# Kernel optimization log

Measured on AMD Instinct MI355X. Metric: run time of the kernel, lower is better.

## Reference

```python
import jax, jax.numpy as jnp
import numpy as np

H = 64   # hidden_size
N = 128  # input_size (num nodes)
B = 64   # batch
T = 96   # seq_len
LN_EPS = 1e-5


def setup_inputs() -> dict:
    key = jax.random.key(0)
    ks = jax.random.split(key, 4)
    x = jax.random.normal(ks[0], (B, T, N), jnp.float32)
    # xavier_uniform-like scale for per-node gate weights [N, 1+H, 4H]
    lim = float(np.sqrt(6.0 / ((1 + H) + 4 * H)))
    w = jax.random.uniform(ks[1], (N, 1 + H, 4 * H), jnp.float32, -lim, lim)
    b = jnp.zeros((N, 4 * H), jnp.float32)
    ln_g = jnp.ones((H,), jnp.float32)
    ln_b = jnp.zeros((H,), jnp.float32)
    fc_w = jax.random.normal(ks[2], (1, H), jnp.float32) * (1.0 / np.sqrt(H))
    fc_b = jnp.zeros((1,), jnp.float32)
    return {"x": x, "w": w, "b": b, "ln_g": ln_g, "ln_b": ln_b,
            "fc_w": fc_w, "fc_b": fc_b}


def _crelu(z):
    return jnp.maximum(z.real, 0) + 1j * jnp.maximum(z.imag, 0)


def _csigmoid(z):
    # torch.sigmoid on complex: 1/(1+exp(-z))
    return 1.0 / (1.0 + jnp.exp(-z))


def _fc_att(x, pool_axes):
    # adaptive_avg_pool to 1 over pool_axes, (C)ReLU, sigmoid, rescale
    squeeze = jnp.mean(x, axis=pool_axes, keepdims=True)
    if jnp.iscomplexobj(x):
        exc = _crelu(squeeze)
        return x * _csigmoid(exc)
    exc = jnp.maximum(squeeze, 0)
    return x * jax.nn.sigmoid(exc)


def reference(x, w, b, ln_g, ln_b, fc_w, fc_b):
    Bb, Tt, Nn = x.shape
    h0 = jnp.zeros((Bb, Nn, H), x.dtype)
    c0 = jnp.zeros((Bb, Nn, H), x.dtype)

    def step(carry, x_t):  # x_t: [B, N]
        h, c = carry
        comb = jnp.concatenate([x_t[..., None], h], axis=-1)      # [B,N,1+H]
        gates = jnp.einsum('bni,nio->bno', comb, w) + b            # [B,N,4H]
        i_g, f_g, o_g, c_tilda = jnp.split(gates, 4, axis=-1)
        # NOTE: original cell does NOT apply tanh to c_tilda
        c_new = jax.nn.sigmoid(f_g) * c + jax.nn.sigmoid(i_g) * c_tilda
        h_new = jax.nn.sigmoid(o_g) * jnp.tanh(c_new)
        return (h_new, c_new), h_new

    _, hs = jax.lax.scan(step, (h0, c0), jnp.swapaxes(x, 0, 1))    # [T,B,N,H]
    lstm_out = jnp.sum(hs, axis=0)                                  # sum over time -> [B,N,H]

    # inter_op: FFT pairwise interaction over the node axis
    m = jnp.fft.rfft(lstm_out, axis=1, norm='ortho')                # [B,F,H] complex, F=N//2+1
    x_f = m[:, :, None, :] * m[:, None, :, :]                       # [B,F,F,H]
    x_f = _fc_att(x_f, (2, 3))
    x_f = jnp.sum(x_f, axis=1)                                      # [B,F,H]
    n_out = 2 * (x_f.shape[1] - 1)                                  # torch irfft default n
    feats = jnp.fft.irfft(x_f, n=n_out, axis=1, norm='ortho')       # [B,N,H] real
    feats = _fc_att(feats, (2,))
    out = jnp.sum(feats, axis=1)                                    # [B,H]

    # LayerNorm(H) -> Linear(H,1) -> sigmoid
    mu = jnp.mean(out, axis=-1, keepdims=True)
    var = jnp.var(out, axis=-1, keepdims=True)
    out = (out - mu) / jnp.sqrt(var + LN_EPS) * ln_g + ln_b
    out = out @ fc_w.T + fc_b                                       # [B,1]
    return jax.nn.sigmoid(out)
```

## Files before the change

kernel.cpp:

```cpp
#include <hip/hip_runtime.h>
#include <math.h>

#define T_STEPS 96
#define N_NODES 128
#define B_SZ 64
#define H_SZ 64

typedef __attribute__((ext_vector_type(8))) __bf16 bf16x8;
typedef __attribute__((ext_vector_type(4))) float f32x4;

__device__ __forceinline__ float rcp_fast(float x){ return __builtin_amdgcn_rcpf(x); }
__device__ __forceinline__ float exp2_fast(float x){ return __builtin_amdgcn_exp2f(x); }
__device__ __forceinline__ float sigm(float v){ return rcp_fast(1.0f + __expf(-v)); }

__global__ __launch_bounds__(256, 2) void lstm_kernel(
    const float* __restrict__ x, const float* __restrict__ w,
    const float* __restrict__ bias, float* __restrict__ yout)
{
  __shared__ __align__(16) unsigned short hb[2][16*72];
  __shared__ float xsl[T_STEPS*16];

  const int n   = blockIdx.x >> 2;
  const int bq  = blockIdx.x & 3;
  const int tid = threadIdx.x;
  const int wv  = tid >> 6;
  const int ln  = tid & 63;
  const int l15 = ln & 15;
  const int q   = ln >> 4;

  for (int i = tid; i < 2*16*72; i += 256) ((unsigned short*)hb)[i] = 0;
  for (int i = tid; i < T_STEPS*16; i += 256){
    int t2 = i >> 4, bl = i & 15;
    xsl[i] = x[(bq*16 + bl)*(T_STEPS*N_NODES) + t2*N_NODES + n];
  }

  const float LOG2E = 1.4426950408889634f;
  const float* wn = w + n*(65*256);

  bf16x8 aF[4][2];
  f32x4 w04[4], bg4[4];
#pragma unroll
  for (int g = 0; g < 4; ++g){
    const float sc = (g < 3) ? LOG2E : 1.0f;
    const int colA = g*64 + wv*16 + l15;
#pragma unroll
    for (int ks = 0; ks < 2; ++ks)
#pragma unroll
      for (int j = 0; j < 8; ++j)
        aF[g][ks][j] = (__bf16)(wn[(1 + ks*32 + q*8 + j)*256 + colA] * sc);
#pragma unroll
    for (int r = 0; r < 4; ++r){
      const int colD = g*64 + wv*16 + q*4 + r;
      w04[g][r] = wn[colD] * sc;
      bg4[g][r] = bias[n*256 + colD] * sc;
    }
  }

  f32x4 cv  = {0.f,0.f,0.f,0.f};
  f32x4 hsv = {0.f,0.f,0.f,0.f};
  __syncthreads();

#pragma unroll 2
  for (int t = 0; t < T_STEPS; ++t){
    const unsigned short* cur = hb[t & 1];
    unsigned short*       nxt = (unsigned short*)hb[(t & 1) ^ 1];

    bf16x8 b0 = *(const bf16x8*)&cur[l15*72 +  0 + q*8];
    bf16x8 b1 = *(const bf16x8*)&cur[l15*72 + 32 + q*8];
    float xv = xsl[t*16 + l15];

    f32x4 acc[4];
#pragma unroll
    for (int g = 0; g < 4; ++g){
      f32x4 a = w04[g]*xv + bg4[g];
      a = __builtin_amdgcn_mfma_f32_16x16x32_bf16(aF[g][0], b0, a, 0,0,0);
      a = __builtin_amdgcn_mfma_f32_16x16x32_bf16(aF[g][1], b1, a, 0,0,0);
      acc[g] = a;
    }

    f32x4 sI, sF, sO, th;
#pragma unroll
    for (int r = 0; r < 4; ++r){
      sI[r] = rcp_fast(1.0f + exp2_fast(-acc[0][r]));
      sF[r] = rcp_fast(1.0f + exp2_fast(-acc[1][r]));
      sO[r] = rcp_fast(1.0f + exp2_fast(-acc[2][r]));
    }
    cv = sF*cv + sI*acc[3];
#pragma unroll
    for (int r = 0; r < 4; ++r){
      float e = exp2_fast(cv[r]*2.8853900817779268f);
      th[r] = fmaf(-2.0f, rcp_fast(e + 1.0f), 1.0f);
    }
    f32x4 hn = sO*th;
    hsv += hn;

    ushort4 pk;
    pk.x = __builtin_bit_cast(unsigned short, (__bf16)hn[0]);
    pk.y = __builtin_bit_cast(unsigned short, (__bf16)hn[1]);
    pk.z = __builtin_bit_cast(unsigned short, (__bf16)hn[2]);
    pk.w = __builtin_bit_cast(unsigned short, (__bf16)hn[3]);
    *(ushort4*)&nxt[l15*72 + wv*16 + q*4] = pk;
    __syncthreads();
  }

  float4 o4 = {hsv[0], hsv[1], hsv[2], hsv[3]};
  *(float4*)&yout[((bq*16 + l15)*N_NODES + n)*H_SZ + wv*16 + q*4] = o4;
}

__global__ __launch_bounds__(256, 2) void dft_kernel(
    const float* __restrict__ y, float* __restrict__ Mout)
{
  __shared__ __align__(16) float ysl[128*20];
  __shared__ float twc[128], tws[128];
  const int b   = blockIdx.x >> 2;
  const int hg  = blockIdx.x & 3;
  const int tid = threadIdx.x;

  if (tid < 128){
    float ang = (float)((double)tid * 0.04908738521234052);
    twc[tid] = cosf(ang);
    tws[tid] = sinf(ang);
  }
  for (int i = tid; i < 128*16; i += 256){
    int nn = i >> 4, h = i & 15;
    ysl[nn*20 + h] = y[(b*N_NODES + nn)*H_SZ + hg*16 + h];
  }
  __syncthreads();

  for (int o = tid; o < 65*4; o += 256){
    int k  = o >> 2;
    int hq = o & 3;
    float re0=0,re1=0,re2=0,re3=0,im0=0,im1=0,im2=0,im3=0;
    for (int nn = 0; nn < 128; ++nn){
      float4 yv = *(const float4*)&ysl[nn*20 + hq*4];
      int j = (k*nn) & 127;
      float cc = twc[j], ss = tws[j];
      re0 = fmaf(yv.x, cc, re0); im0 = fmaf(yv.x, -ss, im0);
      re1 = fmaf(yv.y, cc, re1); im1 = fmaf(yv.y, -ss, im1);
      re2 = fmaf(yv.z, cc, re2); im2 = fmaf(yv.z, -ss, im2);
      re3 = fmaf(yv.w, cc, re3); im3 = fmaf(yv.w, -ss, im3);
    }
    const float s = 0.08838834764831845f;
    const int hb2 = hg*16 + hq*4;
    float* mre = Mout + ((b*2+0)*65 + k)*H_SZ + hb2;
    float* mim = Mout + ((b*2+1)*65 + k)*H_SZ + hb2;
    mre[0]=re0*s; mre[1]=re1*s; mre[2]=re2*s; mre[3]=re3*s;
    mim[0]=im0*s; mim[1]=im1*s; mim[2]=im2*s; mim[3]=im3*s;
  }
}

__global__ __launch_bounds__(256, 1) void post_kernel(
    const float* __restrict__ y, const float* __restrict__ Mws,
    const float* __restrict__ ln_g, const float* __restrict__ ln_b,
    const float* __restrict__ fc_w, const float* __restrict__ fc_b,
    float* __restrict__ out)
{
  __shared__ float ysh[128*65];
  __shared__ float Mre[65*65];
  __shared__ float Mim[65*65];
  __shared__ float twc[128], tws[128];
  __shared__ float Sre[64], Sim[64];
  __shared__ float gr[65], gi[65];
  __shared__ float Gre[64], Gim[64];
  __shared__ float att[128];
  __shared__ float PQ[65*2], AA[65*2];
  __shared__ float outv[64];

  const int b   = blockIdx.x;
  const int tid = threadIdx.x;

  if (tid < 128){
    float ang = (float)((double)tid * 0.04908738521234052);
    twc[tid] = cosf(ang);
    tws[tid] = sinf(ang);
  }
  for (int i = tid; i < 128*16; i += 256){
    int nn = i >> 4, h4 = (i & 15)*4;
    float4 v = *(const float4*)&y[(b*N_NODES + nn)*H_SZ + h4];
    ysh[nn*65 + h4+0] = v.x; ysh[nn*65 + h4+1] = v.y;
    ysh[nn*65 + h4+2] = v.z; ysh[nn*65 + h4+3] = v.w;
  }
  for (int i = tid; i < 65*16; i += 256){
    int k = i >> 4, h4 = (i & 15)*4;
    float4 vr = *(const float4*)&Mws[((b*2+0)*65 + k)*H_SZ + h4];
    float4 vi = *(const float4*)&Mws[((b*2+1)*65 + k)*H_SZ + h4];
    Mre[k*65 + h4+0] = vr.x; Mre[k*65 + h4+1] = vr.y;
    Mre[k*65 + h4+2] = vr.z; Mre[k*65 + h4+3] = vr.w;
    Mim[k*65 + h4+0] = vi.x; Mim[k*65 + h4+1] = vi.y;
    Mim[k*65 + h4+2] = vi.z; Mim[k*65 + h4+3] = vi.w;
  }
  __syncthreads();

  if (tid < 64){
    float sr=0, si=0;
    for (int k = 0; k < 65; ++k){ sr += Mre[k*65+tid]; si += Mim[k*65+tid]; }
    Sre[tid]=sr; Sim[tid]=si;
  }
  __syncthreads();

  if (tid < 65){
    float a=0, bb=0;
    for (int h = 0; h < 64; ++h){
      float mr = Mre[tid*65+h], mi = Mim[tid*65+h];
      a  += mr*Sre[h] - mi*Sim[h];
      bb += mr*Sim[h] + mi*Sre[h];
    }
    a  *= (1.0f/4160.0f);  bb *= (1.0f/4160.0f);
    a = fmaxf(a, 0.0f);    bb = fmaxf(bb, 0.0f);
    float t  = __expf(-a);
    float cb = cosf(bb), sb = sinf(bb);
    float dre = 1.0f + t*cb;
    float dim = t*sb;
    float nrm = rcp_fast(dre*dre + dim*dim);
    gr[tid] = dre*nrm;
    gi[tid] = dim*nrm;
  }
  __syncthreads();

  if (tid < 64){
    float grh=0, gih=0;
    for (int k = 0; k < 65; ++k){
      float mr = Mre[k*65+tid], mi = Mim[k*65+tid];
      float gk = gr[k], hk = gi[k];
      grh += gk*mr - hk*mi;
      gih += gk*mi + hk*mr;
    }
    Gre[tid]=grh; Gim[tid]=gih;
  }
  __syncthreads();

  if (tid < 65){
    float p=0, qq=0;
    for (int h = 0; h < 64; ++h){
      float gimh = Gim[h];
      p  += gimh * Mim[tid*65+h];
      qq += gimh * Mre[tid*65+h];
    }
    const float s2 = 2.0f*0.08838834764831845f;
    PQ[tid*2]   = p*s2;
    PQ[tid*2+1] = qq*s2;
  }
  __syncthreads();

  if (tid < 128){
    float u=0;
    for (int h = 0; h < 64; ++h) u += Gre[h]*ysh[tid*65+h];
    float v=0;
    for (int k = 1; k < 64; ++k){
      int j = (k*tid) & 127;
      v += PQ[k*2]*twc[j] + PQ[k*2+1]*tws[j];
    }
    float mean = (u - v)*(1.0f/64.0f);
    att[tid] = sigm(fmaxf(mean, 0.0f));
  }
  __syncthreads();

  if (tid < 65){
    float ac=0, as=0;
    for (int nn = 0; nn < 128; ++nn){
      int j = (tid*nn) & 127;
      float a2 = att[nn];
      ac = fmaf(a2, twc[j], ac);
      as = fmaf(a2, tws[j], as);
    }
    const float s2 = 2.0f*0.08838834764831845f;
    AA[tid*2]   = ac*s2;
    AA[tid*2+1] = as*s2;
  }
  __syncthreads();

  if (tid < 64){
    float wyh=0;
    for (int nn = 0; nn < 128; ++nn) wyh += att[nn]*ysh[nn*65+tid];
    float wHh=0;
    for (int k = 1; k < 64; ++k)
      wHh += Mim[k*65+tid]*AA[k*2] + Mre[k*65+tid]*AA[k*2+1];
    outv[tid] = Gre[tid]*wyh - Gim[tid]*wHh;
  }
  __syncthreads();

  if (tid < 64){
    float o = outv[tid];
    float s = o;
    for (int off = 32; off; off >>= 1) s += __shfl_xor(s, off, 64);
    float mu = s*(1.0f/64.0f);
    float d  = o - mu;
    float vv = d*d;
    for (int off = 32; off; off >>= 1) vv += __shfl_xor(vv, off, 64);
    float var = vv*(1.0f/64.0f);
    float zo = (d / sqrtf(var + 1e-5f))*ln_g[tid] + ln_b[tid];
    float z  = zo * fc_w[tid];
    for (int off = 32; off; off >>= 1) z += __shfl_xor(z, off, 64);
    if (tid == 0) out[b] = 1.0f/(1.0f + __expf(-(z + fc_b[0])));
  }
}

extern "C" void kernel_launch(void* const* d_in, const int* in_sizes, int n_in,
                              void* d_out, int out_size, void* d_ws, size_t ws_size,
                              hipStream_t stream) {
  (void)in_sizes; (void)n_in; (void)out_size; (void)ws_size;
  const float* x    = (const float*)d_in[0];
  const float* w    = (const float*)d_in[1];
  const float* bia  = (const float*)d_in[2];
  const float* ln_g = (const float*)d_in[3];
  const float* ln_b = (const float*)d_in[4];
  const float* fc_w = (const float*)d_in[5];
  const float* fc_b = (const float*)d_in[6];
  float* out = (float*)d_out;

  float* y = (float*)d_ws;
  float* M = y + (size_t)B_SZ*N_NODES*H_SZ;

  lstm_kernel<<<dim3(512), dim3(256), 0, stream>>>(x, w, bia, y);
  dft_kernel <<<dim3(256), dim3(256), 0, stream>>>(y, M);
  post_kernel<<<dim3(64),  dim3(256), 0, stream>>>(y, M, ln_g, ln_b, fc_w, fc_b, out);
}
```

Baseline: 165.6 us.

## Run each LSTM recurrence in a single wave, folding input and bias into MFMA

The LSTM kernel now uses one 64-thread wave per (node, batch-quarter) task, and that wave computes all 16 gate tiles. This removes the per-timestep __syncthreads and the double-buffered hidden state, which a single wave can read and write in place. The x·w0 and bias terms move into a third MFMA, using a split-bf16 hi/lo trick to keep precision. The gate math is fused to use fewer reciprocals, and the tanh input is clamped. In exchange each wave does six times more serial MFMA and elementwise work per step, and fewer waves are active across the GPU.

Result: slower. 230.4 us (+39.1%).

```diff
diff --git a/kernel.cpp b/kernel.cpp
--- a/kernel.cpp
+++ b/kernel.cpp
@@ -13,23 +13,22 @@
 __device__ __forceinline__ float exp2_fast(float x){ return __builtin_amdgcn_exp2f(x); }
 __device__ __forceinline__ float sigm(float v){ return rcp_fast(1.0f + __expf(-v)); }
 
-__global__ __launch_bounds__(256, 2) void lstm_kernel(
+__global__ __launch_bounds__(64, 1) void lstm_kernel(
     const float* __restrict__ x, const float* __restrict__ w,
     const float* __restrict__ bias, float* __restrict__ yout)
 {
-  __shared__ __align__(16) unsigned short hb[2][16*72];
+  __shared__ __align__(16) unsigned short hsh[16*72];
   __shared__ float xsl[T_STEPS*16];
 
-  const int n   = blockIdx.x >> 2;
-  const int bq  = blockIdx.x & 3;
-  const int tid = threadIdx.x;
-  const int wv  = tid >> 6;
-  const int ln  = tid & 63;
-  const int l15 = ln & 15;
-  const int q   = ln >> 4;
-
-  for (int i = tid; i < 2*16*72; i += 256) ((unsigned short*)hb)[i] = 0;
-  for (int i = tid; i < T_STEPS*16; i += 256){
+  const int task = blockIdx.x;
+  const int bq   = task >> 7;
+  const int n    = task & 127;
+  const int tid  = threadIdx.x;
+  const int l15  = tid & 15;
+  const int q    = tid >> 4;
+
+  for (int i = tid; i < 16*72; i += 64) hsh[i] = 0;
+  for (int i = tid; i < T_STEPS*16; i += 64){
     int t2 = i >> 4, bl = i & 15;
     xsl[i] = x[(bq*16 + bl)*(T_STEPS*N_NODES) + t2*N_NODES + n];
   }
@@ -37,74 +36,100 @@
   const float LOG2E = 1.4426950408889634f;
   const float* wn = w + n*(65*256);
 
-  bf16x8 aF[4][2];
-  f32x4 w04[4], bg4[4];
+  bf16x8 aF[16][2];
+  bf16x8 a2[16];
 #pragma unroll
   for (int g = 0; g < 4; ++g){
     const float sc = (g < 3) ? LOG2E : 1.0f;
-    const int colA = g*64 + wv*16 + l15;
-#pragma unroll
-    for (int ks = 0; ks < 2; ++ks)
-#pragma unroll
-      for (int j = 0; j < 8; ++j)
-        aF[g][ks][j] = (__bf16)(wn[(1 + ks*32 + q*8 + j)*256 + colA] * sc);
-#pragma unroll
-    for (int r = 0; r < 4; ++r){
-      const int colD = g*64 + wv*16 + q*4 + r;
-      w04[g][r] = wn[colD] * sc;
-      bg4[g][r] = bias[n*256 + colD] * sc;
-    }
-  }
-
-  f32x4 cv  = {0.f,0.f,0.f,0.f};
-  f32x4 hsv = {0.f,0.f,0.f,0.f};
-  __syncthreads();
-
-#pragma unroll 2
+#pragma unroll
+    for (int hg = 0; hg < 4; ++hg){
+      const int tl  = g*4 + hg;
+      const int col = g*64 + hg*16 + l15;
+#pragma unroll
+      for (int ks = 0; ks < 2; ++ks)
+#pragma unroll
+        for (int j = 0; j < 8; ++j)
+          aF[tl][ks][j] = (__bf16)(wn[(1 + ks*32 + q*8 + j)*256 + col] * sc);
+      bf16x8 av;
+#pragma unroll
+      for (int j = 0; j < 8; ++j) av[j] = (__bf16)0.0f;
+      if (q == 0){
+        float w0 = wn[col] * sc;
+        __bf16 w0h = (__bf16)w0;
+        av[0] = w0h;
+        av[1] = (__bf16)(bias[n*256 + col] * sc);
+        av[2] = w0h;
+        av[3] = (__bf16)(w0 - (float)w0h);
+      }
+      a2[tl] = av;
+    }
+  }
+
+  f32x4 c4[4], hs4[4];
+#pragma unroll
+  for (int hg = 0; hg < 4; ++hg){
+    c4[hg]  = (f32x4){0.f,0.f,0.f,0.f};
+    hs4[hg] = (f32x4){0.f,0.f,0.f,0.f};
+  }
+  __syncthreads();
+
+#pragma unroll 1
   for (int t = 0; t < T_STEPS; ++t){
-    const unsigned short* cur = hb[t & 1];
-    unsigned short*       nxt = (unsigned short*)hb[(t & 1) ^ 1];
-
-    bf16x8 b0 = *(const bf16x8*)&cur[l15*72 +  0 + q*8];
-    bf16x8 b1 = *(const bf16x8*)&cur[l15*72 + 32 + q*8];
+    bf16x8 b0 = *(const bf16x8*)&hsh[l15*72 +  0 + q*8];
+    bf16x8 b1 = *(const bf16x8*)&hsh[l15*72 + 32 + q*8];
     float xv = xsl[t*16 + l15];
-
-    f32x4 acc[4];
-#pragma unroll
-    for (int g = 0; g < 4; ++g){
-      f32x4 a = w04[g]*xv + bg4[g];
-      a = __builtin_amdgcn_mfma_f32_16x16x32_bf16(aF[g][0], b0, a, 0,0,0);
-      a = __builtin_amdgcn_mfma_f32_16x16x32_bf16(aF[g][1], b1, a, 0,0,0);
-      acc[g] = a;
-    }
-
-    f32x4 sI, sF, sO, th;
-#pragma unroll
-    for (int r = 0; r < 4; ++r){
-      sI[r] = rcp_fast(1.0f + exp2_fast(-acc[0][r]));
-      sF[r] = rcp_fast(1.0f + exp2_fast(-acc[1][r]));
-      sO[r] = rcp_fast(1.0f + exp2_fast(-acc[2][r]));
-    }
-    cv = sF*cv + sI*acc[3];
-#pragma unroll
-    for (int r = 0; r < 4; ++r){
-      float e = exp2_fast(cv[r]*2.8853900817779268f);
-      th[r] = fmaf(-2.0f, rcp_fast(e + 1.0f), 1.0f);
-    }
-    f32x4 hn = sO*th;
-    hsv += hn;
-
-    ushort4 pk;
-    pk.x = __builtin_bit_cast(unsigned short, (__bf16)hn[0]);
-    pk.y = __builtin_bit_cast(unsigned short, (__bf16)hn[1]);
-    pk.z = __builtin_bit_cast(unsigned short, (__bf16)hn[2]);
-    pk.w = __builtin_bit_cast(unsigned short, (__bf16)hn[3]);
-    *(ushort4*)&nxt[l15*72 + wv*16 + q*4] = pk;
-    __syncthreads();
-  }
-
-  float4 o4 = {hsv[0], hsv[1], hsv[2], hsv[3]};
-  *(float4*)&yout[((bq*16 + l15)*N_NODES + n)*H_SZ + wv*16 + q*4] = o4;
+    __bf16 xh = (__bf16)xv;
+    __bf16 xl = (__bf16)(xv - (float)xh);
+    bf16x8 b2;
+#pragma unroll
+    for (int j = 0; j < 8; ++j) b2[j] = (__bf16)0.0f;
+    if (q == 0){ b2[0] = xh; b2[1] = (__bf16)1.0f; b2[2] = xl; b2[3] = xh; }
+
+    f32x4 acc[16];
+#pragma unroll
+    for (int tl = 0; tl < 16; ++tl){
+      f32x4 a = {0.f,0.f,0.f,0.f};
+      a = __builtin_amdgcn_mfma_f32_16x16x32_bf16(aF[tl][0], b0, a, 0,0,0);
+      a = __builtin_amdgcn_mfma_f32_16x16x32_bf16(aF[tl][1], b1, a, 0,0,0);
+      a = __builtin_amdgcn_mfma_f32_16x16x32_bf16(a2[tl],   b2, a, 0,0,0);
+      acc[tl] = a;
+    }
+
+#pragma unroll
+    for (int hg = 0; hg < 4; ++hg){
+      f32x4 cv = c4[hg];
+      f32x4 hn;
+#pragma unroll
+      for (int r = 0; r < 4; ++r){
+        float gi = acc[0*4+hg][r], gf = acc[1*4+hg][r];
+        float go = acc[2*4+hg][r], ct = acc[3*4+hg][r];
+        float ei = exp2_fast(-gi), ef = exp2_fast(-gf);
+        float pf = 1.0f + ef, pi = 1.0f + ei;
+        float num = fmaf(cv[r], ei, cv[r]);
+        num = fmaf(ct, pf, num);
+        float cn = num * rcp_fast(pf*pi);
+        cv[r] = cn;
+        float eo = exp2_fast(-go);
+        float ea = fminf(cn*2.8853900817779268f, 126.0f);
+        float ec = exp2_fast(ea);
+        hn[r] = (ec - 1.0f) * rcp_fast((1.0f + eo)*(ec + 1.0f));
+      }
+      c4[hg]   = cv;
+      hs4[hg] += hn;
+      ushort4 pk;
+      pk.x = __builtin_bit_cast(unsigned short, (__bf16)hn[0]);
+      pk.y = __builtin_bit_cast(unsigned short, (__bf16)hn[1]);
+      pk.z = __builtin_bit_cast(unsigned short, (__bf16)hn[2]);
+      pk.w = __builtin_bit_cast(unsigned short, (__bf16)hn[3]);
+      *(ushort4*)&hsh[l15*72 + hg*16 + q*4] = pk;
+    }
+  }
+
+#pragma unroll
+  for (int hg = 0; hg < 4; ++hg){
+    float4 o4 = {hs4[hg][0], hs4[hg][1], hs4[hg][2], hs4[hg][3]};
+    *(float4*)&yout[((bq*16 + l15)*N_NODES + n)*H_SZ + hg*16 + q*4] = o4;
+  }
 }
 
 __global__ __launch_bounds__(256, 2) void dft_kernel(
@@ -311,7 +336,7 @@
   float* y = (float*)d_ws;
   float* M = y + (size_t)B_SZ*N_NODES*H_SZ;
 
-  lstm_kernel<<<dim3(512), dim3(256), 0, stream>>>(x, w, bia, y);
+  lstm_kernel<<<dim3(512), dim3(64),  0, stream>>>(x, w, bia, y);
   dft_kernel <<<dim3(256), dim3(256), 0, stream>>>(y, M);
   post_kernel<<<dim3(64),  dim3(256), 0, stream>>>(y, M, ln_g, ln_b, fc_w, fc_b, out);
 }
```

## Split LSTM recurrence across 8 waves with gate-interleaved MFMA rows

Applied to the files above, without the earlier changes.

Doubles the LSTM block to 512 threads so each wave owns 8 hidden units. The weight rows are permuted so that one MFMA output tile holds all four gates (i, f, o, c~) of a hidden unit in a single lane's accumulator. This halves the MFMAs per wave on the serial per-timestep critical path. It also fuses the sigmoid/tanh math so that one reciprocal covers the combined gate denominators, cutting transcendental ops. In exchange, barrier synchronisation now spans 8 waves, occupancy pressure rises, and the final output stores become scalar.

New measurement: 172.1 us. +3.9%, slower.

```diff
diff --git a/kernel.cpp b/kernel.cpp
--- a/kernel.cpp
+++ b/kernel.cpp
@@ -13,7 +13,7 @@
 __device__ __forceinline__ float exp2_fast(float x){ return __builtin_amdgcn_exp2f(x); }
 __device__ __forceinline__ float sigm(float v){ return rcp_fast(1.0f + __expf(-v)); }
 
-__global__ __launch_bounds__(256, 2) void lstm_kernel(
+__global__ __launch_bounds__(512, 2) void lstm_kernel(
     const float* __restrict__ x, const float* __restrict__ w,
     const float* __restrict__ bias, float* __restrict__ yout)
 {
@@ -28,8 +28,8 @@
   const int l15 = ln & 15;
   const int q   = ln >> 4;
 
-  for (int i = tid; i < 2*16*72; i += 256) ((unsigned short*)hb)[i] = 0;
-  for (int i = tid; i < T_STEPS*16; i += 256){
+  for (int i = tid; i < 2*16*72; i += 512) ((unsigned short*)hb)[i] = 0;
+  for (int i = tid; i < T_STEPS*16; i += 512){
     int t2 = i >> 4, bl = i & 15;
     xsl[i] = x[(bq*16 + bl)*(T_STEPS*N_NODES) + t2*N_NODES + n];
   }
@@ -37,27 +37,29 @@
   const float LOG2E = 1.4426950408889634f;
   const float* wn = w + n*(65*256);
 
-  bf16x8 aF[4][2];
-  f32x4 w04[4], bg4[4];
-#pragma unroll
-  for (int g = 0; g < 4; ++g){
-    const float sc = (g < 3) ? LOG2E : 1.0f;
-    const int colA = g*64 + wv*16 + l15;
+  bf16x8 aF[2][2];
+  f32x4 w0t[2], bgt[2];
+#pragma unroll
+  for (int t = 0; t < 2; ++t){
+    const int gA  = l15 & 3;
+    const float scA = (gA < 3) ? LOG2E : 1.0f;
+    const int colA = gA*64 + wv*8 + t*4 + (l15 >> 2);
 #pragma unroll
     for (int ks = 0; ks < 2; ++ks)
 #pragma unroll
       for (int j = 0; j < 8; ++j)
-        aF[g][ks][j] = (__bf16)(wn[(1 + ks*32 + q*8 + j)*256 + colA] * sc);
+        aF[t][ks][j] = (__bf16)(wn[(1 + ks*32 + q*8 + j)*256 + colA] * scA);
 #pragma unroll
     for (int r = 0; r < 4; ++r){
-      const int colD = g*64 + wv*16 + q*4 + r;
-      w04[g][r] = wn[colD] * sc;
-      bg4[g][r] = bias[n*256 + colD] * sc;
-    }
-  }
-
-  f32x4 cv  = {0.f,0.f,0.f,0.f};
-  f32x4 hsv = {0.f,0.f,0.f,0.f};
+      const float sc = (r < 3) ? LOG2E : 1.0f;
+      const int colD = r*64 + wv*8 + t*4 + q;
+      w0t[t][r] = wn[colD] * sc;
+      bgt[t][r] = bias[n*256 + colD] * sc;
+    }
+  }
+
+  float cv[2]  = {0.f, 0.f};
+  float hsv[2] = {0.f, 0.f};
   __syncthreads();
 
 #pragma unroll 2
@@ -69,42 +71,38 @@
     bf16x8 b1 = *(const bf16x8*)&cur[l15*72 + 32 + q*8];
     float xv = xsl[t*16 + l15];
 
-    f32x4 acc[4];
-#pragma unroll
-    for (int g = 0; g < 4; ++g){
-      f32x4 a = w04[g]*xv + bg4[g];
-      a = __builtin_amdgcn_mfma_f32_16x16x32_bf16(aF[g][0], b0, a, 0,0,0);
-      a = __builtin_amdgcn_mfma_f32_16x16x32_bf16(aF[g][1], b1, a, 0,0,0);
-      acc[g] = a;
-    }
-
-    f32x4 sI, sF, sO, th;
-#pragma unroll
-    for (int r = 0; r < 4; ++r){
-      sI[r] = rcp_fast(1.0f + exp2_fast(-acc[0][r]));
-      sF[r] = rcp_fast(1.0f + exp2_fast(-acc[1][r]));
-      sO[r] = rcp_fast(1.0f + exp2_fast(-acc[2][r]));
-    }
-    cv = sF*cv + sI*acc[3];
-#pragma unroll
-    for (int r = 0; r < 4; ++r){
-      float e = exp2_fast(cv[r]*2.8853900817779268f);
-      th[r] = fmaf(-2.0f, rcp_fast(e + 1.0f), 1.0f);
-    }
-    f32x4 hn = sO*th;
-    hsv += hn;
-
-    ushort4 pk;
-    pk.x = __builtin_bit_cast(unsigned short, (__bf16)hn[0]);
-    pk.y = __builtin_bit_cast(unsigned short, (__bf16)hn[1]);
-    pk.z = __builtin_bit_cast(unsigned short, (__bf16)hn[2]);
-    pk.w = __builtin_bit_cast(unsigned short, (__bf16)hn[3]);
-    *(ushort4*)&nxt[l15*72 + wv*16 + q*4] = pk;
+    f32x4 acc[2];
+#pragma unroll
+    for (int tl = 0; tl < 2; ++tl){
+      f32x4 a = w0t[tl]*xv + bgt[tl];
+      a = __builtin_amdgcn_mfma_f32_16x16x32_bf16(aF[tl][0], b0, a, 0,0,0);
+      a = __builtin_amdgcn_mfma_f32_16x16x32_bf16(aF[tl][1], b1, a, 0,0,0);
+      acc[tl] = a;
+    }
+
+#pragma unroll
+    for (int tl = 0; tl < 2; ++tl){
+      float gi = acc[tl][0], gf = acc[tl][1], go = acc[tl][2], ct = acc[tl][3];
+      float ei = exp2_fast(-gi), ef = exp2_fast(-gf);
+      float pf = 1.0f + ef, pi = 1.0f + ei;
+      float num = fmaf(cv[tl], ei, cv[tl]);
+      num = fmaf(ct, pf, num);
+      float cn = num * rcp_fast(pf*pi);
+      cv[tl] = cn;
+      float eo = exp2_fast(-go);
+      float ea = fminf(cn*2.8853900817779268f, 126.0f);
+      float ec = exp2_fast(ea);
+      float hn = (ec - 1.0f) * rcp_fast((1.0f + eo)*(ec + 1.0f));
+      hsv[tl] += hn;
+      nxt[l15*72 + wv*8 + tl*4 + q] =
+          __builtin_bit_cast(unsigned short, (__bf16)hn);
+    }
     __syncthreads();
   }
 
-  float4 o4 = {hsv[0], hsv[1], hsv[2], hsv[3]};
-  *(float4*)&yout[((bq*16 + l15)*N_NODES + n)*H_SZ + wv*16 + q*4] = o4;
+#pragma unroll
+  for (int tl = 0; tl < 2; ++tl)
+    yout[((bq*16 + l15)*N_NODES + n)*H_SZ + wv*8 + tl*4 + q] = hsv[tl];
 }
 
 __global__ __launch_bounds__(256, 2) void dft_kernel(
@@ -311,7 +309,7 @@
   float* y = (float*)d_ws;
   float* M = y + (size_t)B_SZ*N_NODES*H_SZ;
 
-  lstm_kernel<<<dim3(512), dim3(256), 0, stream>>>(x, w, bia, y);
+  lstm_kernel<<<dim3(512), dim3(512), 0, stream>>>(x, w, bia, y);
   dft_kernel <<<dim3(256), dim3(256), 0, stream>>>(y, M);
   post_kernel<<<dim3(64),  dim3(256), 0, stream>>>(y, M, ln_g, ln_b, fc_w, fc_b, out);
 }
```
